# Kernel optimization log

Measured on AMD Instinct MI355X. Metric: run time of the kernel, lower is better.

## Reference

```python
import jax, jax.numpy as jnp
import numpy as np

B, S, D, H = 4, 2048, 1024, 16
HD = D // H  # head_dim = 64


def setup_inputs() -> dict:
    key = jax.random.key(0)
    ks = jax.random.split(key, 5)
    scale = 1.0 / np.sqrt(D)  # xavier-ish
    return {
        "query": jax.random.normal(ks[0], (B, S, D), dtype=jnp.float32),
        "Wq": jax.random.normal(ks[1], (D, D), dtype=jnp.float32) * scale,
        "bq": jnp.zeros((D,), dtype=jnp.float32),
        "Wk": jax.random.normal(ks[2], (D, D), dtype=jnp.float32) * scale,
        "bk": jnp.zeros((D,), dtype=jnp.float32),
        "Wv": jax.random.normal(ks[3], (D, D), dtype=jnp.float32) * scale,
        "bv": jnp.zeros((D,), dtype=jnp.float32),
        "Wo": jax.random.normal(ks[4], (D, D), dtype=jnp.float32) * scale,
        "bo": jnp.zeros((D,), dtype=jnp.float32),
    }


def reference(query, Wq, bq, Wk, bk, Wv, bv, Wo, bo):
    # Self-attention: key = value = query. Linear layers use y = x @ W^T + b (torch nn.Linear).
    q = query @ Wq.T + bq
    k = query @ Wk.T + bk
    v = query @ Wv.T + bv
    # [B, S, D] -> [B, H, S, HD]
    q = q.reshape(B, S, H, HD).transpose(0, 2, 1, 3)
    k = k.reshape(B, S, H, HD).transpose(0, 2, 1, 3)
    v = v.reshape(B, S, H, HD).transpose(0, 2, 1, 3)
    scores = jnp.einsum('bhqd,bhkd->bhqk', q, k) / jnp.sqrt(jnp.float32(HD))
    attn = jax.nn.softmax(scores, axis=-1)  # dropout=0 (eval)
    out = jnp.einsum('bhqk,bhkd->bhqd', attn, v)
    out = out.transpose(0, 2, 1, 3).reshape(B, S, D)
    out = out @ Wo.T + bo
    return out
```

## Files before the change

### kernel.cpp

```cpp
#include <hip/hip_runtime.h>
#include <cstdint>


#define B_ 4
#define S_ 2048
#define D_ 1024
#define H_ 16
#define HD_ 64
#define QKV_N 3072
#define QK_LD 2048
#define SCALE_Q 0.18033688011111772f

typedef __bf16 bf16x8 __attribute__((ext_vector_type(8)));
typedef __bf16 bf16x2 __attribute__((ext_vector_type(2)));
typedef float f32x4 __attribute__((ext_vector_type(4)));
typedef short short8 __attribute__((ext_vector_type(8)));

__device__ __forceinline__ unsigned short f2bf(float f) {
  unsigned int u = __builtin_bit_cast(unsigned int, f);
  u = (u + 0x7FFFu + ((u >> 16) & 1u)) >> 16;
  return (unsigned short)u;
}

__device__ __forceinline__ unsigned int pkbf(float a, float b) {
  bf16x2 v;
  v.x = (__bf16)a;
  v.y = (__bf16)b;
  return __builtin_bit_cast(unsigned int, v);
}

__device__ __forceinline__ void gload16(const void* g, void* l) {
  __builtin_amdgcn_global_load_lds(
      (const __attribute__((address_space(1))) void*)g,
      (__attribute__((address_space(3))) void*)l, 16, 0, 0);
}

__global__ __launch_bounds__(256) void cvt_all(
    const float* __restrict__ x, const float* __restrict__ w0, const float* __restrict__ w1,
    const float* __restrict__ w2, const float* __restrict__ w3,
    const float* __restrict__ bq, const float* __restrict__ bk, const float* __restrict__ bv,
    unsigned short* __restrict__ xb, unsigned short* __restrict__ wcat,
    float* __restrict__ bcat) {
  const int blk = blockIdx.x;
  const int t = threadIdx.x;
  if (blk < 4096) {
    size_t i = (size_t)blk * 256 + t;
    const float4* p = (const float4*)x + i * 2;
    float4 a = p[0], b = p[1];
    unsigned short o[8] = {f2bf(a.x), f2bf(a.y), f2bf(a.z), f2bf(a.w),
                           f2bf(b.x), f2bf(b.y), f2bf(b.z), f2bf(b.w)};
    *(uint4*)(xb + i * 8) = *(const uint4*)o;
  } else if (blk < 6144) {
    int y = (blk - 4096) >> 9;
    const float* src = (y == 0) ? w0 : (y == 1) ? w1 : (y == 2) ? w2 : w3;
    float s = (y == 0) ? SCALE_Q : 1.0f;
    size_t i = (size_t)((blk - 4096) & 511) * 256 + t;
    const float4* p = (const float4*)src + i * 2;
    float4 a = p[0], b = p[1];
    unsigned short o[8] = {f2bf(a.x * s), f2bf(a.y * s), f2bf(a.z * s), f2bf(a.w * s),
                           f2bf(b.x * s), f2bf(b.y * s), f2bf(b.z * s), f2bf(b.w * s)};
    *(uint4*)(wcat + (size_t)y * 1048576 + i * 8) = *(const uint4*)o;
  } else {
    for (int i = t; i < 3072; i += 256) {
      float v = (i < 1024) ? bq[i] * SCALE_Q : (i < 2048) ? bk[i - 1024] : bv[i - 2048];
      bcat[i] = v;
    }
  }
}

#define SBAR() __builtin_amdgcn_sched_barrier(0)
#define BARRIER()                      \
  do {                                 \
    SBAR();                            \
    __builtin_amdgcn_s_barrier();      \
    SBAR();                            \
  } while (0)
#define WAITLGKM()                                      \
  do {                                                  \
    asm volatile("s_waitcnt lgkmcnt(0)" ::: "memory");  \
    SBAR();                                             \
  } while (0)

__device__ __forceinline__ void ld_af2(const unsigned short* s, int rowbase, int quad,
                                       int sw, bf16x8 af[2][2]) {
#pragma unroll
  for (int mi2 = 0; mi2 < 2; ++mi2) {
    int row = rowbase + mi2 * 16;
#pragma unroll
    for (int kk = 0; kk < 2; ++kk)
      af[mi2][kk] = *(const bf16x8*)&s[row * 64 + ((((kk << 2) + quad) ^ sw) << 3)];
  }
}

__device__ __forceinline__ void ld_bf3(const unsigned short* s, int rowbase, int quad,
                                       int sw, bf16x8 bf[3][2]) {
#pragma unroll
  for (int ni2 = 0; ni2 < 3; ++ni2) {
    int row = rowbase + ni2 * 16;
#pragma unroll
    for (int kk = 0; kk < 2; ++kk)
      bf[ni2][kk] = *(const bf16x8*)&s[row * 64 + ((((kk << 2) + quad) ^ sw) << 3)];
  }
}

#define MMQ(qm, half, BF)                                                                \
  _Pragma("unroll") for (int mi2 = 0; mi2 < 2; ++mi2)                                    \
  _Pragma("unroll") for (int ni2 = 0; ni2 < 3; ++ni2)                                    \
  _Pragma("unroll") for (int kk = 0; kk < 2; ++kk)                                       \
      acc[(qm) * 2 + mi2][(half) * 3 + ni2] = __builtin_amdgcn_mfma_f32_16x16x32_bf16(   \
          af[mi2][kk], BF[ni2][kk], acc[(qm) * 2 + mi2][(half) * 3 + ni2], 0, 0, 0);

__global__ __launch_bounds__(512, 2) void gemm_qkv_384(
    const unsigned short* __restrict__ A, const unsigned short* __restrict__ W,
    const float* __restrict__ bias, unsigned short* __restrict__ qk,
    unsigned short* __restrict__ vt) {
  __shared__ __attribute__((aligned(16))) unsigned short sA[2][128 * 64];
  __shared__ __attribute__((aligned(16))) unsigned short sB[2][384 * 64];

  const int t = threadIdx.x;
  const int lane = t & 63;
  const int w = t >> 6;
  const int lm = lane & 15;
  const int quad = lane >> 4;
  const int sw = lm & 7;
  const int wm = (w >> 2) * 64;
  const int wn = (w & 3) * 96;

  const int bid = blockIdx.x;
  const int xcd = bid & 7, lin = bid >> 3;
  const int mt = xcd * 8 + (lin & 7);
  const int nt = lin >> 3;
  const int m0 = mt * 128, n0 = nt * 384;
  const int K = 1024;

  const int srow = t >> 3;
  const int scol = ((t & 7) ^ ((t >> 3) & 7)) << 3;
  const unsigned short* Ab = A + ((size_t)m0 + srow) * K + scol;
  const unsigned short* Wb = W + ((size_t)n0 + srow) * K + scol;

#define QSTG_A(bb, q, kt) gload16(Ab + (size_t)((q) * 64) * K + (kt), &sA[bb][(q) * 4096 + w * 512])
#define QSTG_B(bb, q, kt) gload16(Wb + (size_t)((q) * 64) * K + (kt), &sB[bb][(q) * 4096 + w * 512])

  QSTG_A(0, 0, 0); QSTG_A(0, 1, 0);
  QSTG_B(0, 0, 0); QSTG_B(0, 1, 0); QSTG_B(0, 2, 0);
  QSTG_B(0, 3, 0); QSTG_B(0, 4, 0); QSTG_B(0, 5, 0);
  QSTG_B(1, 0, 64); QSTG_B(1, 1, 64);
  QSTG_A(1, 0, 64); QSTG_A(1, 1, 64);
  QSTG_B(1, 2, 64); QSTG_B(1, 3, 64);
  asm volatile("s_waitcnt vmcnt(6)" ::: "memory");
  BARRIER();

  f32x4 acc[4][6] = {};
  bf16x8 af[2][2], bf0[3][2], bf1[3][2];

#define QGROUP(c, kn1, kn2)                                                           \
  do {                                                                                \
    ld_af2(sA[c], wm + lm, quad, sw, af);                                             \
    ld_bf3(sB[c], wn + lm, quad, sw, bf0);                                            \
    QSTG_B(c ^ 1, 4, kn1);                                                            \
    QSTG_B(c ^ 1, 5, kn1);                                                            \
    BARRIER(); WAITLGKM();                                                            \
    __builtin_amdgcn_s_setprio(1); MMQ(0, 0, bf0); __builtin_amdgcn_s_setprio(0);     \
    BARRIER();                                                                        \
    ld_bf3(sB[c], wn + 48 + lm, quad, sw, bf1);                                       \
    BARRIER(); WAITLGKM();                                                            \
    __builtin_amdgcn_s_setprio(1); MMQ(0, 1, bf1); __builtin_amdgcn_s_setprio(0);     \
    BARRIER();                                                                        \
    ld_af2(sA[c], wm + 32 + lm, quad, sw, af);                                        \
    QSTG_B(c, 0, kn2);                                                                \
    QSTG_B(c, 1, kn2);                                                                \
    BARRIER(); WAITLGKM();                                                            \
    __builtin_amdgcn_s_setprio(1); MMQ(1, 0, bf0); __builtin_amdgcn_s_setprio(0);     \
    BARRIER();                                                                        \
    QSTG_A(c, 0, kn2);                                                                \
    QSTG_A(c, 1, kn2);                                                                \
    QSTG_B(c, 2, kn2);                                                                \
    QSTG_B(c, 3, kn2);                                                                \
    asm volatile("s_waitcnt vmcnt(6)" ::: "memory");                                  \
    BARRIER();                                                                        \
    __builtin_amdgcn_s_setprio(1); MMQ(1, 1, bf1); __builtin_amdgcn_s_setprio(0);     \
    BARRIER();                                                                        \
  } while (0)

  for (int kt = 0; kt < K; kt += 128) {
    const int kn1a = kt + 64;
    const int kn2a = (kt + 128 < K) ? kt + 128 : K - 64;
    const int kn1b = kn2a;
    const int kn2b = (kt + 192 < K) ? kt + 192 : K - 64;
    QGROUP(0, kn1a, kn2a);
    QGROUP(1, kn1b, kn2b);
  }

  asm volatile("s_waitcnt vmcnt(0)" ::: "memory");

#pragma unroll
  for (int mi = 0; mi < 4; ++mi) {
    const int rbase = m0 + wm + mi * 16 + quad * 4;
#pragma unroll
    for (int ni = 0; ni < 6; ++ni) {
      const int col = n0 + wn + ni * 16 + lm;
      const float bv = bias[col];
      float v0 = acc[mi][ni][0] + bv, v1 = acc[mi][ni][1] + bv;
      float v2 = acc[mi][ni][2] + bv, v3 = acc[mi][ni][3] + bv;
      if (col < 2048) {
        qk[(size_t)(rbase + 0) * QK_LD + col] = f2bf(v0);
        qk[(size_t)(rbase + 1) * QK_LD + col] = f2bf(v1);
        qk[(size_t)(rbase + 2) * QK_LD + col] = f2bf(v2);
        qk[(size_t)(rbase + 3) * QK_LD + col] = f2bf(v3);
      } else {
        int c2 = col - 2048;
        int bh = (m0 >> 11) * 16 + (c2 >> 6);
        int hd = c2 & 63;
        int sbase = rbase & 2047;
        uint2 pk = {pkbf(v0, v1), pkbf(v2, v3)};
        *(uint2*)(vt + (size_t)bh * (HD_ * S_) + (size_t)hd * S_ + sbase) = pk;
      }
    }
  }
}

__global__ __launch_bounds__(256) void gemm_bt(
    const unsigned short* __restrict__ A, const unsigned short* __restrict__ W,
    const float* __restrict__ bias, void* __restrict__ Cout,
    unsigned short* __restrict__ vt, int M, int N, int K, int mode) {
  __shared__ __attribute__((aligned(16))) unsigned short sA[128 * 32];
  __shared__ __attribute__((aligned(16))) unsigned short sB[128 * 32];
  const int t = threadIdx.x;
  const int lane = t & 63;
  const int w = t >> 6;
  const int lm = lane & 15;
  const int quad = lane >> 4;
  const int m0 = blockIdx.x * 128;
  const int n0 = blockIdx.y * 128;
  const int wm = (w & 1) * 64;
  const int wn = (w >> 1) * 64;

  const int off0 = t * 8, off1 = t * 8 + 2048;
  const int ar0 = off0 >> 5, ac0 = (((off0 >> 3) & 3) ^ ((ar0 >> 1) & 3)) * 8;
  const int ar1 = off1 >> 5, ac1 = (((off1 >> 3) & 3) ^ ((ar1 >> 1) & 3)) * 8;
  const unsigned short* Ag0 = A + (size_t)(m0 + ar0) * K + ac0;
  const unsigned short* Ag1 = A + (size_t)(m0 + ar1) * K + ac1;
  const unsigned short* Wg0 = W + (size_t)(n0 + ar0) * K + ac0;
  const unsigned short* Wg1 = W + (size_t)(n0 + ar1) * K + ac1;
  unsigned short* sA0 = &sA[w * 512];
  unsigned short* sA1 = &sA[2048 + w * 512];
  unsigned short* sB0 = &sB[w * 512];
  unsigned short* sB1 = &sB[2048 + w * 512];

  f32x4 acc[4][4] = {};

  for (int kt = 0; kt < K; kt += 32) {
    gload16(Ag0 + kt, sA0);
    gload16(Ag1 + kt, sA1);
    gload16(Wg0 + kt, sB0);
    gload16(Wg1 + kt, sB1);
    __syncthreads();
    bf16x8 af[4], bf[4];
#pragma unroll
    for (int mi = 0; mi < 4; ++mi) {
      int row = wm + mi * 16 + lm;
      af[mi] = *(const bf16x8*)&sA[row * 32 + ((quad ^ ((row >> 1) & 3)) << 3)];
    }
#pragma unroll
    for (int ni = 0; ni < 4; ++ni) {
      int row = wn + ni * 16 + lm;
      bf[ni] = *(const bf16x8*)&sB[row * 32 + ((quad ^ ((row >> 1) & 3)) << 3)];
    }
#pragma unroll
    for (int mi = 0; mi < 4; ++mi)
#pragma unroll
      for (int ni = 0; ni < 4; ++ni)
        acc[mi][ni] = __builtin_amdgcn_mfma_f32_16x16x32_bf16(af[mi], bf[ni], acc[mi][ni], 0, 0, 0);
    __syncthreads();
  }

#pragma unroll
  for (int mi = 0; mi < 4; ++mi)
#pragma unroll
    for (int ni = 0; ni < 4; ++ni) {
      int col = n0 + wn + ni * 16 + lm;
      float bv = bias[col];
      float v0 = acc[mi][ni][0] + bv, v1 = acc[mi][ni][1] + bv;
      float v2 = acc[mi][ni][2] + bv, v3 = acc[mi][ni][3] + bv;
      int rbase = m0 + wm + mi * 16 + quad * 4;
      if (mode == 0) {
        float* op = (float*)Cout;
        op[(size_t)(rbase + 0) * N + col] = v0;
        op[(size_t)(rbase + 1) * N + col] = v1;
        op[(size_t)(rbase + 2) * N + col] = v2;
        op[(size_t)(rbase + 3) * N + col] = v3;
      } else if (col < 2048) {
        unsigned short* op = (unsigned short*)Cout;
        op[(size_t)(rbase + 0) * QK_LD + col] = f2bf(v0);
        op[(size_t)(rbase + 1) * QK_LD + col] = f2bf(v1);
        op[(size_t)(rbase + 2) * QK_LD + col] = f2bf(v2);
        op[(size_t)(rbase + 3) * QK_LD + col] = f2bf(v3);
      } else {
        int c = col - 2048;
        int bh = (m0 >> 11) * 16 + (c >> 6);
        int hd = c & 63;
        int sbase = (rbase & 2047);
        uint2 pk = {pkbf(v0, v1), pkbf(v2, v3)};
        *(uint2*)(vt + (size_t)bh * (HD_ * S_) + (size_t)hd * S_ + sbase) = pk;
      }
    }
}

__global__ __launch_bounds__(512, 4) void attn_kernel(
    const unsigned short* __restrict__ qk, const unsigned short* __restrict__ vt,
    unsigned short* __restrict__ ab) {
  __shared__ __attribute__((aligned(16))) unsigned short sK[2][64 * 64];
  __shared__ __attribute__((aligned(16))) unsigned short sV[2][64 * 64];
  __shared__ __attribute__((aligned(16))) unsigned short sP[8][32 * 64];

  const int t = threadIdx.x;
  const int lane = t & 63;
  const int w = t >> 6;
  const int lm = lane & 15;
  const int quad = lane >> 4;
  const int bh = blockIdx.x & 63;
  const int b = bh >> 4, h = bh & 15;
  const int q0 = (blockIdx.x >> 6) * 256;

  const unsigned short* qg = qk + (size_t)b * S_ * QK_LD + h * HD_;
  const unsigned short* kg = qg + 1024;
  const unsigned short* vg = vt + (size_t)bh * HD_ * S_;

  const int r0 = t >> 3;
  const int c0 = ((t & 7) ^ (r0 & 7)) * 8;

  gload16(kg + (size_t)r0 * QK_LD + c0, &sK[0][w * 512]);
  gload16(vg + (size_t)r0 * S_ + c0, &sV[0][w * 512]);

  bf16x8 qf[2][2];
#pragma unroll
  for (int mi = 0; mi < 2; ++mi) {
    int row = q0 + w * 32 + mi * 16 + lm;
#pragma unroll
    for (int kc = 0; kc < 2; ++kc)
      qf[mi][kc] = *(const bf16x8*)(qg + (size_t)row * QK_LD + kc * 32 + quad * 8);
  }
  __syncthreads();

  unsigned short* sPw = sP[w];
  const bf16x8 ones = __builtin_bit_cast(bf16x8, (short8)(short)0x3F80);
  f32x4 o[2][4] = {};
  f32x4 Lacc[2] = {};

  for (int n0 = 0; n0 < S_; n0 += 64) {
    const int cur = (n0 >> 6) & 1, nxt = cur ^ 1;
    if (n0 + 64 < S_) {
      gload16(kg + (size_t)(n0 + 64 + r0) * QK_LD + c0, &sK[nxt][w * 512]);
      gload16(vg + (size_t)r0 * S_ + (n0 + 64) + c0, &sV[nxt][w * 512]);
    }

    f32x4 s[2][4] = {};
#pragma unroll
    for (int kc = 0; kc < 2; ++kc)
#pragma unroll
      for (int nb = 0; nb < 4; ++nb) {
        int row = nb * 16 + lm;
        bf16x8 kf = *(const bf16x8*)&sK[cur][row * 64 + (((kc * 4 + quad) ^ (row & 7)) << 3)];
#pragma unroll
        for (int mi = 0; mi < 2; ++mi)
          s[mi][nb] = __builtin_amdgcn_mfma_f32_16x16x32_bf16(kf, qf[mi][kc], s[mi][nb], 0, 0, 0);
      }

#pragma unroll
    for (int mi = 0; mi < 2; ++mi) {
      int prow = mi * 16 + lm;
      char* rowp = (char*)sPw + prow * 128;
#pragma unroll
      for (int nb = 0; nb < 4; ++nb) {
        const f32x4& sv = s[mi][nb];
        uint2 pk = {pkbf(__builtin_amdgcn_exp2f(sv[0]), __builtin_amdgcn_exp2f(sv[1])),
                    pkbf(__builtin_amdgcn_exp2f(sv[2]), __builtin_amdgcn_exp2f(sv[3]))};
        int c16 = (nb * 2 + (quad >> 1)) ^ (prow & 7);
        *(uint2*)(rowp + (c16 << 4) + ((quad & 1) << 3)) = pk;
      }
    }

#pragma unroll
    for (int kc = 0; kc < 2; ++kc) {
      bf16x8 pf[2];
#pragma unroll
      for (int mi = 0; mi < 2; ++mi) {
        int prow = mi * 16 + lm;
        pf[mi] = *(const bf16x8*)&sPw[prow * 64 + (((kc * 4 + quad) ^ (prow & 7)) << 3)];
        Lacc[mi] = __builtin_amdgcn_mfma_f32_16x16x32_bf16(pf[mi], ones, Lacc[mi], 0, 0, 0);
      }
#pragma unroll
      for (int nf = 0; nf < 4; ++nf) {
        int row = nf * 16 + lm;
        bf16x8 vf = *(const bf16x8*)&sV[cur][row * 64 + (((kc * 4 + quad) ^ (row & 7)) << 3)];
#pragma unroll
        for (int mi = 0; mi < 2; ++mi)
          o[mi][nf] = __builtin_amdgcn_mfma_f32_16x16x32_bf16(pf[mi], vf, o[mi][nf], 0, 0, 0);
      }
    }
    __syncthreads();
  }

#pragma unroll
  for (int mi = 0; mi < 2; ++mi)
#pragma unroll
    for (int r = 0; r < 4; ++r) {
      float rinv = 1.0f / Lacc[mi][r];
      int row = q0 + w * 32 + mi * 16 + quad * 4 + r;
#pragma unroll
      for (int nf = 0; nf < 4; ++nf) {
        int col = h * HD_ + nf * 16 + lm;
        ab[(size_t)(b * S_ + row) * D_ + col] = f2bf(o[mi][nf][r] * rinv);
      }
    }
}

extern "C" void kernel_launch(void* const* d_in, const int* in_sizes, int n_in,
                              void* d_out, int out_size, void* d_ws, size_t ws_size,
                              hipStream_t stream) {
  const float* x = (const float*)d_in[0];
  const float* Wq = (const float*)d_in[1];
  const float* bq = (const float*)d_in[2];
  const float* Wk = (const float*)d_in[3];
  const float* bk = (const float*)d_in[4];
  const float* Wv = (const float*)d_in[5];
  const float* bv = (const float*)d_in[6];
  const float* Wo = (const float*)d_in[7];
  const float* bo = (const float*)d_in[8];
  float* out = (float*)d_out;

  const size_t E = (size_t)B_ * S_ * D_;
  const size_t WE = (size_t)D_ * D_;
  unsigned short* xb = (unsigned short*)d_ws;
  unsigned short* wcat = xb + E;
  unsigned short* wob = wcat + 3 * WE;
  float* bcat = (float*)(wcat + 4 * WE);
  unsigned short* qkb = (unsigned short*)(bcat + 4096);
  unsigned short* vtb = qkb + (size_t)B_ * S_ * QK_LD;
  unsigned short* abuf = xb;

  cvt_all<<<dim3(6145), 256, 0, stream>>>(x, Wq, Wk, Wv, Wo, bq, bk, bv, xb, wcat, bcat);

  gemm_qkv_384<<<dim3(512), 512, 0, stream>>>(xb, wcat, bcat, qkb, vtb);
  attn_kernel<<<dim3(512), 512, 0, stream>>>(qkb, vtb, abuf);
  gemm_bt<<<dim3((B_ * S_) / 128, D_ / 128), 256, 0, stream>>>(
      abuf, wob, bo, out, nullptr, B_ * S_, D_, D_, 0);
}
```

Measured before the change: 261.5 us.

## Software-pipeline attention loop so QK^T of next tile overlaps softmax and PV

The attention inner loop is unrolled by two with ping-pong score registers. The QK^T MFMAs for tile i+1 are issued before the exp/pack and PV MFMAs of tile i, with K and V prefetches interleaved around the barriers. The goal is to hide exp and LDS latency behind matrix work and to expose more instruction-level parallelism. The cost is a second set of score accumulators, which raises register pressure and may lower occupancy. It also adds an explicit lgkmcnt wait before the PV step.

```diff
diff --git a/kernel.cpp b/kernel.cpp
--- a/kernel.cpp
+++ b/kernel.cpp
@@ -329,8 +329,11 @@
   const int r0 = t >> 3;
   const int c0 = ((t & 7) ^ (r0 & 7)) * 8;
 
-  gload16(kg + (size_t)r0 * QK_LD + c0, &sK[0][w * 512]);
-  gload16(vg + (size_t)r0 * S_ + c0, &sV[0][w * 512]);
+#define PFK(ti) gload16(kg + (size_t)((ti) * 64 + r0) * QK_LD + c0, &sK[(ti) & 1][w * 512])
+#define PFV(ti) gload16(vg + (size_t)r0 * S_ + (ti) * 64 + c0, &sV[(ti) & 1][w * 512])
+
+  PFK(0);
+  PFV(0);
 
   bf16x8 qf[2][2];
 #pragma unroll
@@ -346,60 +349,83 @@
   const bf16x8 ones = __builtin_bit_cast(bf16x8, (short8)(short)0x3F80);
   f32x4 o[2][4] = {};
   f32x4 Lacc[2] = {};
-
-  for (int n0 = 0; n0 < S_; n0 += 64) {
-    const int cur = (n0 >> 6) & 1, nxt = cur ^ 1;
-    if (n0 + 64 < S_) {
-      gload16(kg + (size_t)(n0 + 64 + r0) * QK_LD + c0, &sK[nxt][w * 512]);
-      gload16(vg + (size_t)r0 * S_ + (n0 + 64) + c0, &sV[nxt][w * 512]);
-    }
-
-    f32x4 s[2][4] = {};
-#pragma unroll
-    for (int kc = 0; kc < 2; ++kc)
-#pragma unroll
-      for (int nb = 0; nb < 4; ++nb) {
-        int row = nb * 16 + lm;
-        bf16x8 kf = *(const bf16x8*)&sK[cur][row * 64 + (((kc * 4 + quad) ^ (row & 7)) << 3)];
-#pragma unroll
-        for (int mi = 0; mi < 2; ++mi)
-          s[mi][nb] = __builtin_amdgcn_mfma_f32_16x16x32_bf16(kf, qf[mi][kc], s[mi][nb], 0, 0, 0);
-      }
-
-#pragma unroll
-    for (int mi = 0; mi < 2; ++mi) {
-      int prow = mi * 16 + lm;
-      char* rowp = (char*)sPw + prow * 128;
-#pragma unroll
-      for (int nb = 0; nb < 4; ++nb) {
-        const f32x4& sv = s[mi][nb];
-        uint2 pk = {pkbf(__builtin_amdgcn_exp2f(sv[0]), __builtin_amdgcn_exp2f(sv[1])),
-                    pkbf(__builtin_amdgcn_exp2f(sv[2]), __builtin_amdgcn_exp2f(sv[3]))};
-        int c16 = (nb * 2 + (quad >> 1)) ^ (prow & 7);
-        *(uint2*)(rowp + (c16 << 4) + ((quad & 1) << 3)) = pk;
-      }
-    }
-
-#pragma unroll
-    for (int kc = 0; kc < 2; ++kc) {
-      bf16x8 pf[2];
-#pragma unroll
-      for (int mi = 0; mi < 2; ++mi) {
-        int prow = mi * 16 + lm;
-        pf[mi] = *(const bf16x8*)&sPw[prow * 64 + (((kc * 4 + quad) ^ (prow & 7)) << 3)];
-        Lacc[mi] = __builtin_amdgcn_mfma_f32_16x16x32_bf16(pf[mi], ones, Lacc[mi], 0, 0, 0);
-      }
-#pragma unroll
-      for (int nf = 0; nf < 4; ++nf) {
-        int row = nf * 16 + lm;
-        bf16x8 vf = *(const bf16x8*)&sV[cur][row * 64 + (((kc * 4 + quad) ^ (row & 7)) << 3)];
-#pragma unroll
-        for (int mi = 0; mi < 2; ++mi)
-          o[mi][nf] = __builtin_amdgcn_mfma_f32_16x16x32_bf16(pf[mi], vf, o[mi][nf], 0, 0, 0);
-      }
-    }
+  f32x4 sE[2][4], sO[2][4];
+
+#define QKM(ci, S)                                                                        \
+  do {                                                                                    \
+    _Pragma("unroll") for (int mi = 0; mi < 2; ++mi)                                      \
+    _Pragma("unroll") for (int nb = 0; nb < 4; ++nb)                                      \
+        S[mi][nb] = (f32x4){0.0f, 0.0f, 0.0f, 0.0f};                                      \
+    _Pragma("unroll") for (int kc = 0; kc < 2; ++kc)                                      \
+    _Pragma("unroll") for (int nb = 0; nb < 4; ++nb) {                                    \
+      int row = nb * 16 + lm;                                                             \
+      bf16x8 kf = *(const bf16x8*)&sK[ci][row * 64 + (((kc * 4 + quad) ^ (row & 7)) << 3)]; \
+      _Pragma("unroll") for (int mi = 0; mi < 2; ++mi)                                    \
+        S[mi][nb] = __builtin_amdgcn_mfma_f32_16x16x32_bf16(kf, qf[mi][kc], S[mi][nb], 0, 0, 0); \
+    }                                                                                     \
+  } while (0)
+
+#define SMW(S)                                                                            \
+  do {                                                                                    \
+    _Pragma("unroll") for (int mi = 0; mi < 2; ++mi) {                                    \
+      int prow = mi * 16 + lm;                                                            \
+      char* rowp = (char*)sPw + prow * 128;                                               \
+      _Pragma("unroll") for (int nb = 0; nb < 4; ++nb) {                                  \
+        const f32x4& sv = S[mi][nb];                                                      \
+        uint2 pk = {pkbf(__builtin_amdgcn_exp2f(sv[0]), __builtin_amdgcn_exp2f(sv[1])),   \
+                    pkbf(__builtin_amdgcn_exp2f(sv[2]), __builtin_amdgcn_exp2f(sv[3]))};  \
+        int c16 = (nb * 2 + (quad >> 1)) ^ (prow & 7);                                    \
+        *(uint2*)(rowp + (c16 << 4) + ((quad & 1) << 3)) = pk;                            \
+      }                                                                                   \
+    }                                                                                     \
+  } while (0)
+
+#define PVM(pi)                                                                           \
+  do {                                                                                    \
+    asm volatile("s_waitcnt lgkmcnt(0)" ::: "memory");                                    \
+    _Pragma("unroll") for (int kc = 0; kc < 2; ++kc) {                                    \
+      bf16x8 pf[2];                                                                       \
+      _Pragma("unroll") for (int mi = 0; mi < 2; ++mi) {                                  \
+        int prow = mi * 16 + lm;                                                          \
+        pf[mi] = *(const bf16x8*)&sPw[prow * 64 + (((kc * 4 + quad) ^ (prow & 7)) << 3)]; \
+        Lacc[mi] = __builtin_amdgcn_mfma_f32_16x16x32_bf16(pf[mi], ones, Lacc[mi], 0, 0, 0); \
+      }                                                                                   \
+      _Pragma("unroll") for (int nf = 0; nf < 4; ++nf) {                                  \
+        int row = nf * 16 + lm;                                                           \
+        bf16x8 vf = *(const bf16x8*)&sV[pi][row * 64 + (((kc * 4 + quad) ^ (row & 7)) << 3)]; \
+        _Pragma("unroll") for (int mi = 0; mi < 2; ++mi)                                  \
+          o[mi][nf] = __builtin_amdgcn_mfma_f32_16x16x32_bf16(pf[mi], vf, o[mi][nf], 0, 0, 0); \
+      }                                                                                   \
+    }                                                                                     \
+  } while (0)
+
+  QKM(0, sE);
+  PFK(1);
+  __syncthreads();
+  PFV(1);
+
+  for (int k = 0; k < 15; ++k) {
+    const int i1 = 2 * k + 1;
+    QKM(1, sO);
+    PFK(i1 + 1);
+    SMW(sE);
+    PVM(0);
     __syncthreads();
-  }
+    PFV(i1 + 1);
+    QKM(0, sE);
+    PFK(i1 + 2);
+    SMW(sO);
+    PVM(1);
+    __syncthreads();
+    PFV(i1 + 2);
+  }
+
+  QKM(1, sO);
+  SMW(sE);
+  PVM(0);
+  __syncthreads();
+  SMW(sO);
+  PVM(1);
 
 #pragma unroll
   for (int mi = 0; mi < 2; ++mi)
```

After: 373.8 us. +43.0%, slower.
